# Kernel tuning notes

Hardware: AMD Instinct MI355X
Metric: run time of the kernel (lower is better)

## Reference

```python
import jax, jax.numpy as jnp
import numpy as np

B, L, C = 32, 1024, 32     # batch, seq_len, enc_in
D = 512                     # d_model / hidden_size
SEG = 16                    # seg_len
K = 25                      # moving_avg kernel
SX = L // SEG               # seg_num_x = 64 sequential GRU steps
PRED = 16                   # pred_len == seg_len -> seg_num_y = 1


def setup_inputs() -> dict:
    key = jax.random.key(0)
    ks = jax.random.split(key, 20)
    r = lambda i, shape: jax.random.normal(ks[i], shape, dtype=jnp.float32) * 0.05
    return {
        "x": jax.random.normal(ks[0], (B, L, C), dtype=jnp.float32),
        "W_emb": r(1, (D, SEG)), "b_emb": r(2, (D,)),
        "Wih_s": r(3, (3 * D, D)), "Whh_s": r(4, (3 * D, D)),
        "bih_s": r(5, (3 * D,)), "bhh_s": r(6, (3 * D,)),
        "Wih_t": r(7, (3 * D, D)), "Whh_t": r(8, (3 * D, D)),
        "bih_t": r(9, (3 * D,)), "bhh_t": r(10, (3 * D,)),
        "pos_s": r(11, (1, D // 2)), "ch_s": r(12, (C, D // 2)),
        "pos_t": r(13, (1, D // 2)), "ch_t": r(14, (C, D // 2)),
        "Wps": r(15, (SEG, D)), "bps": r(16, (SEG,)),
        "Wpt": r(17, (SEG, D)), "bpt": r(18, (SEG,)),
    }


def _moving_mean(x, k):
    # Autoformer moving_avg over dim 1 with edge replication (length preserved, k odd)
    pad = (k - 1) // 2
    xp = jnp.concatenate([jnp.repeat(x[:, :1], pad, 1), x, jnp.repeat(x[:, -1:], pad, 1)], axis=1)
    cs = jnp.cumsum(xp, axis=1)
    cs = jnp.concatenate([jnp.zeros_like(cs[:, :1]), cs], axis=1)
    return (cs[:, k:] - cs[:, :-k]) / k


def _gru_cell(x, h, Wih, Whh, bih, bhh):
    gi = x @ Wih.T + bih
    gh = h @ Whh.T + bhh
    ir, iz, in_ = jnp.split(gi, 3, axis=-1)
    hr, hz, hn = jnp.split(gh, 3, axis=-1)
    r = jax.nn.sigmoid(ir + hr)
    z = jax.nn.sigmoid(iz + hz)
    n = jnp.tanh(in_ + r * hn)
    return (1.0 - z) * n + z * h


def _forward(x, W_emb, b_emb, Wih_s, Whh_s, bih_s, bhh_s, Wih_t, Whh_t, bih_t, bhh_t,
             pos_s, ch_s, pos_t, ch_t, Wps, bps, Wpt, bpt):
    seq_last = jax.lax.stop_gradient(x[:, -1:, :])          # (B,1,C), detached
    xc = (x - seq_last).transpose(0, 2, 1)                  # (B,C,L)
    mean = _moving_mean(xc, K)                              # trend
    xs = xc - mean                                          # seasonal residual
    xt = mean
    # value embedding: (B*C, SX, SEG) -> (B*C, SX, D), ReLU
    xs = jax.nn.relu(xs.reshape(-1, SX, SEG) @ W_emb.T + b_emb)
    xt = jax.nn.relu(xt.reshape(-1, SX, SEG) @ W_emb.T + b_emb)
    N = B * C
    h0 = jnp.zeros((N, D), x.dtype)

    def step(carry, inp):
        hs, ht = carry
        xs_i, xt_i = inp
        hs = _gru_cell(xs_i, hs, Wih_s, Whh_s, bih_s, bhh_s)
        ht = _gru_cell(xt_i, ht, Wih_t, Whh_t, bih_t, bhh_t)
        return (hs, ht), None

    (hs, ht), _ = jax.lax.scan(step, (h0, h0), (xs.transpose(1, 0, 2), xt.transpose(1, 0, 2)))

    # decoder (seg_num_y == 1): pos/channel embedding -> one more GRUCell step
    pe_s = jnp.tile(jnp.concatenate([jnp.broadcast_to(pos_s, (C, D // 2)), ch_s], -1), (B, 1))  # (B*C,D)
    pe_t = jnp.tile(jnp.concatenate([jnp.broadcast_to(pos_t, (C, D // 2)), ch_t], -1), (B, 1))
    hs2 = _gru_cell(pe_s, hs, Wih_s, Whh_s, bih_s, bhh_s)
    ht2 = _gru_cell(pe_t, ht, Wih_t, Whh_t, bih_t, bhh_t)
    # predict heads (dropout is identity in eval)
    y = ht2 @ Wpt.T + bpt + hs2 @ Wps.T + bps               # (B*C, SEG)
    y = y.reshape(B, C, PRED).transpose(0, 2, 1)            # (B, PRED, C)
    return y + seq_last


def reference(x, W_emb, b_emb, Wih_s, Whh_s, bih_s, bhh_s, Wih_t, Whh_t, bih_t, bhh_t,
              pos_s, ch_s, pos_t, ch_t, Wps, bps, Wpt, bpt):
    return _forward(x, W_emb, b_emb, Wih_s, Whh_s, bih_s, bhh_s, Wih_t, Whh_t, bih_t, bhh_t,
                    pos_s, ch_s, pos_t, ch_t, Wps, bps, Wpt, bpt)
```

## Files before the change

kernel.cpp:

```cpp
#include <hip/hip_runtime.h>
#include <math.h>

#define B_   32
#define L_   1024
#define C_   32
#define D_   512
#define SEG_ 16
#define SX_  64
#define N_   1024

typedef _Float16 f16x8 __attribute__((ext_vector_type(8)));
typedef _Float16 f16x4 __attribute__((ext_vector_type(4)));
typedef float    f32x4 __attribute__((ext_vector_type(4)));

__device__ __forceinline__ void stage16(const void* g, void* l) {
    __builtin_amdgcn_global_load_lds((const __attribute__((address_space(1))) void*)g,
                                     (__attribute__((address_space(3))) void*)l, 16, 0, 0);
}
__device__ __forceinline__ void stage16l(const void* g, void* l) {
    __builtin_amdgcn_global_load_lds((const __attribute__((address_space(1))) void*)g,
                                     (__attribute__((address_space(3))) void*)l, 16, 0, 1);
}
__device__ __forceinline__ void store_v4_sc0(void* p, f16x8 v) {
    asm volatile("global_store_dwordx4 %0, %1, off sc0" :: "v"(p), "v"(v) : "memory");
}
__device__ __forceinline__ float fsig(float x) {
    return __builtin_amdgcn_rcpf(1.f + __expf(-x));
}
__device__ __forceinline__ float ftanh(float x) {
    return 1.f - 2.f * __builtin_amdgcn_rcpf(1.f + __expf(2.f * x));
}

__global__ __launch_bounds__(256) void prep_kernel(const float* __restrict__ x,
                                                   float* __restrict__ xs_seg,
                                                   float* __restrict__ xt_seg) {
    int b = blockIdx.x >> 2;
    int t = ((blockIdx.x & 3) << 8) + threadIdx.x;
    const float* xb    = x + (size_t)b * (L_ * C_);
    const float* xrow  = xb + (size_t)t * C_;
    const float* xlast = xb + (size_t)(L_ - 1) * C_;

    float diff[C_];
#pragma unroll
    for (int c = 0; c < C_; ++c) diff[c] = xrow[c] - xlast[c];
    float ps[C_ + 1];
    ps[0] = 0.f;
#pragma unroll
    for (int c = 0; c < C_; ++c) ps[c + 1] = ps[c] + diff[c];

    int s = t >> 4, q = t & 15;
#pragma unroll
    for (int c = 0; c < C_; ++c) {
        int lo = c - 12, hi = c + 12;
        float sum = ps[(hi < 31 ? hi : 31) + 1] - ps[lo > 0 ? lo : 0];
        if (lo < 0)  sum += (float)(-lo)     * diff[0];
        if (hi > 31) sum += (float)(hi - 31) * diff[31];
        float mean = sum * (1.0f / 25.0f);
        size_t idx = ((size_t)s * N_ + (size_t)(b * C_ + c)) * SEG_ + q;
        xt_seg[idx] = mean;
        xs_seg[idx] = diff[c] - mean;
    }
}

__global__ __launch_bounds__(256) void emb_kernel(
    const float* __restrict__ xs_seg, const float* __restrict__ xt_seg,
    const float* __restrict__ W_emb, const float* __restrict__ b_emb,
    _Float16* __restrict__ emb_buf, int s0) {
    int bid = blockIdx.x;
    int gru = bid >> 8, sl = (bid >> 4) & 15, nch = bid & 15;
    int step = s0 + sl, n0 = nch * 64;
    const float* xseg = gru ? xt_seg : xs_seg;
    __shared__ float xl[64 * 16];
    int tid = threadIdx.x;
    const float* src = xseg + ((size_t)step * N_ + n0) * SEG_;
    for (int i = tid; i < 1024; i += 256) xl[i] = src[i];

    int kg = tid & 127;
    int rh = tid >> 7;
    float w[4][16], bb[4];
#pragma unroll
    for (int i = 0; i < 4; ++i) {
        int k = kg * 4 + i;
        const float4* wr = (const float4*)(W_emb + (size_t)k * 16);
#pragma unroll
        for (int v = 0; v < 4; ++v) {
            float4 tt = wr[v];
            w[i][v * 4 + 0] = tt.x; w[i][v * 4 + 1] = tt.y;
            w[i][v * 4 + 2] = tt.z; w[i][v * 4 + 3] = tt.w;
        }
        bb[i] = b_emb[k];
    }
    __syncthreads();
    _Float16* dst = emb_buf + ((size_t)(sl * 2 + gru) * N_ + n0) * D_ + kg * 4;
    for (int r = 0; r < 32; ++r) {
        int row = rh * 32 + r;
        float a0 = bb[0], a1 = bb[1], a2 = bb[2], a3 = bb[3];
#pragma unroll
        for (int q = 0; q < 16; ++q) {
            float xv = xl[row * 16 + q];
            a0 = fmaf(xv, w[0][q], a0);
            a1 = fmaf(xv, w[1][q], a1);
            a2 = fmaf(xv, w[2][q], a2);
            a3 = fmaf(xv, w[3][q], a3);
        }
        f16x4 v;
        v[0] = (_Float16)(a0 > 0.f ? a0 : 0.f);
        v[1] = (_Float16)(a1 > 0.f ? a1 : 0.f);
        v[2] = (_Float16)(a2 > 0.f ? a2 : 0.f);
        v[3] = (_Float16)(a3 > 0.f ? a3 : 0.f);
        *(f16x4*)(dst + (size_t)row * D_) = v;
    }
}

__global__ __launch_bounds__(256) void pack_wih_kernel(
    const float* __restrict__ Wih_s, const float* __restrict__ Wih_t,
    _Float16* __restrict__ wp) {
    int e = blockIdx.x * 256 + threadIdx.x;
    int kk = e & 31;
    int t = e >> 5;
    int gc = t % 1536;
    int t2 = t / 1536;
    int kt = t2 & 15, gru = t2 >> 4;
    int member = gc / 192, r = gc % 192;
    int wn = r / 48, r2 = r % 48;
    int gate = r2 >> 4, jl = r2 & 15;
    int j = member * 64 + wn * 16 + jl;
    int k = kt * 32 + kk;
    const float* W = gru ? Wih_t : Wih_s;
    wp[e] = (_Float16)W[(size_t)(gate * 512 + j) * 512 + k];
}

__global__ __launch_bounds__(256) void pack_whh5_kernel(
    const float* __restrict__ Whh_s, const float* __restrict__ Whh_t,
    _Float16* __restrict__ wp) {
    int e = blockIdx.x * 256 + threadIdx.x;
    int fi = e & 7;
    int t = e >> 3;
    int c = t % 3072;
    int t2 = t / 3072;
    int kt = t2 & 3;
    int t3 = t2 >> 2;
    int member = t3 & 7, gru = t3 >> 3;
    int gc = c >> 4, s = c & 15;
    int q = s ^ (gc & 15);
    int k = kt * 128 + q * 8 + fi;
    int wn = gc / 48, r2 = gc % 48;
    int gate = r2 >> 4, jl = r2 & 15;
    int j = member * 64 + wn * 16 + jl;
    const float* W = gru ? Whh_t : Whh_s;
    wp[e] = (_Float16)W[(size_t)(gate * 512 + j) * 512 + k];
}

__global__ __launch_bounds__(256) void pack_pe_kernel(
    const float* __restrict__ pos_s, const float* __restrict__ ch_s,
    const float* __restrict__ pos_t, const float* __restrict__ ch_t,
    _Float16* __restrict__ pe) {
    int e = blockIdx.x * 256 + threadIdx.x;
    int k = e & 511;
    int n = (e >> 9) & 1023;
    int gru = e >> 19;
    int c = n & 31;
    const float* pos = gru ? pos_t : pos_s;
    const float* ch  = gru ? ch_t  : ch_s;
    float v = (k < 256) ? pos[k] : ch[c * 256 + (k - 256)];
    pe[e] = (_Float16)v;
}

__global__ __launch_bounds__(512, 2) void gi_gemm_kernel(
    const _Float16* __restrict__ emb, const _Float16* __restrict__ pe,
    const _Float16* __restrict__ wih_pack,
    _Float16* __restrict__ gi, _Float16* __restrict__ gi_pe, int mode) {
    __shared__ __align__(16) char smem[53248];
    char* sA = smem;
    char* sB = smem + 8192;
    int Mt = blockIdx.x & 7, Nt = blockIdx.x >> 3;
    int sl = blockIdx.y, gru = blockIdx.z;
    int tid = threadIdx.x, w = tid >> 6, lane = tid & 63;
    int wm = w & 1, wn = w >> 1, ml = lane & 15, qq = lane >> 4;

    const char* Ab = mode ? (const char*)(pe  + (size_t)gru * N_ * D_)
                          : (const char*)(emb + (size_t)(sl * 2 + gru) * N_ * D_);
    const char* Bb = (const char*)wih_pack + (size_t)gru * 16 * 1536 * 64
                     + (size_t)Nt * 192 * 64;

    int rA = tid >> 2, kqA = (tid & 3) ^ ((rA >> 1) & 3);
    const char* gA = Ab + (size_t)(Mt * 128 + rA) * 1024 + kqA * 16;
    int g1 = tid >> 2, kq1 = (tid & 3) ^ ((g1 >> 1) & 3);
    int c2 = 512 + tid, g2 = c2 >> 2, kq2 = (c2 & 3) ^ ((g2 >> 1) & 3);

    int offA[4], offB[3];
#pragma unroll
    for (int mf = 0; mf < 4; ++mf) {
        int row = wm * 64 + mf * 16 + ml;
        offA[mf] = (row * 4 + (qq ^ ((row >> 1) & 3))) * 16;
    }
#pragma unroll
    for (int g = 0; g < 3; ++g) {
        int gc = wn * 48 + g * 16 + ml;
        offB[g] = (gc * 4 + (qq ^ ((gc >> 1) & 3))) * 16;
    }

    f32x4 acc[4][3];
#pragma unroll
    for (int mf = 0; mf < 4; ++mf)
#pragma unroll
        for (int g = 0; g < 3; ++g) {
            f32x4 z = {0.f, 0.f, 0.f, 0.f};
            acc[mf][g] = z;
        }

    for (int kt = 0; kt < 16; ++kt) {
        __syncthreads();
        stage16(gA + kt * 64, sA + w * 1024);
        const char* Bkt = Bb + (size_t)kt * (1536 * 64);
        stage16(Bkt + g1 * 64 + kq1 * 16, sB + w * 1024);
        if (w < 4) stage16(Bkt + g2 * 64 + kq2 * 16, sB + 8192 + w * 1024);
        asm volatile("s_waitcnt vmcnt(0)" ::: "memory");
        __syncthreads();
        f16x8 a[4];
#pragma unroll
        for (int mf = 0; mf < 4; ++mf) a[mf] = *(const f16x8*)(sA + offA[mf]);
#pragma unroll
        for (int g = 0; g < 3; ++g) {
            f16x8 b = *(const f16x8*)(sB + offB[g]);
#pragma unroll
            for (int mf = 0; mf < 4; ++mf)
                acc[mf][g] = __builtin_amdgcn_mfma_f32_16x16x32_f16(a[mf], b, acc[mf][g], 0, 0, 0);
        }
    }

    __syncthreads();
#pragma unroll
    for (int mf = 0; mf < 4; ++mf) {
        int wm_c = mf >> 1, rt = mf & 1;
        int tid_c = (wn * 2 + wm_c) * 64 + qq * 16 + ml;
        char* base = smem + wm * 26624 + tid_c * 52;
#pragma unroll
        for (int g = 0; g < 3; ++g)
#pragma unroll
            for (int reg = 0; reg < 4; ++reg) {
                int v = rt * 12 + reg * 3 + g;
                *(_Float16*)(base + v * 2) = (_Float16)acc[mf][g][reg];
            }
    }
    __syncthreads();
    _Float16* ob = mode ? gi_pe + (size_t)gru * 8 * 16 * 512 * 24
                        : gi    + (size_t)(sl * 2 + gru) * 8 * 16 * 512 * 24;
    char* obB = (char*)ob;
#pragma unroll
    for (int s = 0; s < 6; ++s) {
        int o = tid * 16 + s * 8192;
        int mc = o / 24576;
        int o2 = o - mc * 24576;
        int tc = o2 / 48;
        int r  = o2 - tc * 48;
        const char* src = smem + mc * 26624 + tc * 52 + r;
        int4 val;
        val.x = *(const int*)(src);
        val.y = *(const int*)(src + 4);
        val.z = *(const int*)(src + 8);
        val.w = *(const int*)(src + 12);
        *(int4*)(obB + (size_t)(Nt * 16 + Mt * 2 + mc) * 24576 + o2) = val;
    }
}

__global__ __launch_bounds__(512) void gru_chain_kernel(
    const _Float16* __restrict__ whh_pk5,
    const _Float16* __restrict__ gi_base,
    const float* __restrict__ bih_s, const float* __restrict__ bhh_s,
    const float* __restrict__ bih_t, const float* __restrict__ bhh_t,
    _Float16* __restrict__ hbf0, _Float16* __restrict__ hbf1,
    unsigned* __restrict__ flags, int nsteps, int sbase) {
    __shared__ __align__(16) char sA[65536];
    __shared__ __align__(16) char sEx[49152];
    int bid = blockIdx.x;
    int member = bid >> 5, chain = bid & 31;
    int Mt = chain & 15, gru = chain >> 4;
    int tid = threadIdx.x, w = tid >> 6, lane = tid & 63;
    int ml = lane & 15, qq = lane >> 4;
    int km = w & 1, wn = w >> 1;

    const char* h0 = (const char*)hbf0 + ((size_t)gru * N_ + Mt * 64) * 1024;
    const char* h1 = (const char*)hbf1 + ((size_t)gru * N_ + Mt * 64) * 1024;

    f16x8 bfr[3][8];
    {
        const _Float16* Wb = whh_pk5 + (size_t)(gru * 8 + member) * 4 * 24576;
#pragma unroll
        for (int g = 0; g < 3; ++g) {
            int gc = wn * 48 + g * 16 + ml;
#pragma unroll
            for (int ks = 0; ks < 8; ++ks) {
                int kt = km * 2 + (ks >> 2);
                int q8 = ((ks & 3) * 4 + qq) ^ (gc & 15);
                bfr[g][ks] = *(const f16x8*)(Wb + (size_t)kt * 24576
                                             + (size_t)(gc * 16 + q8) * 8);
            }
        }
    }

    int cS0 = (lane & 48) | ((lane & 15) ^ (w & 15));
    int cS1 = (lane & 48) | ((lane & 15) ^ ((w + 8) & 15));

    int offR[4], cp[8];
#pragma unroll
    for (int rt = 0; rt < 4; ++rt) offR[rt] = (rt * 16 + ml) * 1024;
#pragma unroll
    for (int ks = 0; ks < 8; ++ks) {
        int c = km * 32 + ks * 4 + qq;
        cp[ks] = ((c & 48) | ((c & 15) ^ ml)) * 16;
    }

    const float* bi = gru ? bih_t : bih_s;
    const float* bh = gru ? bhh_t : bhh_s;
    int j = member * 64 + wn * 16 + ml;
    float bir = bi[j], biz = bi[D_ + j], bin = bi[2 * D_ + j];
    float bhr = bh[j], bhz = bh[D_ + j], bhn = bh[2 * D_ + j];
    float hp[2][4];
#pragma unroll
    for (int rtL = 0; rtL < 2; ++rtL)
#pragma unroll
        for (int reg = 0; reg < 4; ++reg) {
            int row = Mt * 64 + km * 32 + rtL * 16 + qq * 4 + reg;
            hp[rtL][reg] = (float)hbf0[((size_t)gru * N_ + row) * D_ + j];
        }

    unsigned* fbase = flags + chain * 256;
    const _Float16* giTid0 = gi_base
        + (((size_t)gru * 8 + member) * 16 + Mt) * 512 * 24 + (size_t)tid * 24;
    size_t giStep = (size_t)2 * 8 * 16 * 512 * 24;

    int dir0 = sbase & 1;
    f16x8 gv0, gv1, gv2;
    {
        const _Float16* gp = giTid0;
        gv0 = *(const f16x8*)(gp);
        gv1 = *(const f16x8*)(gp + 8);
        gv2 = *(const f16x8*)(gp + 16);
        const char* hin = dir0 ? h1 : h0;
#pragma unroll
        for (int r = 0; r < 8; ++r) {
            int row = r * 8 + w;
            stage16l(hin + (size_t)row * 1024 + (size_t)((r & 1) ? cS1 : cS0) * 16,
                     sA + row * 1024);
        }
    }

    for (int it = 0; it < nsteps; ++it) {
        int gstep = sbase + it;
        _Float16* hout = (gstep & 1) ? hbf0 : hbf1;

        f32x4 acc[4][3];
#pragma unroll
        for (int rt = 0; rt < 4; ++rt)
#pragma unroll
            for (int g = 0; g < 3; ++g) {
                f32x4 z = {0.f, 0.f, 0.f, 0.f};
                acc[rt][g] = z;
            }

        asm volatile("s_waitcnt vmcnt(0)" ::: "memory");
        __syncthreads();

#pragma unroll
        for (int ks = 0; ks < 8; ++ks) {
            f16x8 a0 = *(const f16x8*)(sA + offR[0] + cp[ks]);
            f16x8 a1 = *(const f16x8*)(sA + offR[1] + cp[ks]);
            f16x8 a2 = *(const f16x8*)(sA + offR[2] + cp[ks]);
            f16x8 a3 = *(const f16x8*)(sA + offR[3] + cp[ks]);
#pragma unroll
            for (int g = 0; g < 3; ++g) {
                acc[0][g] = __builtin_amdgcn_mfma_f32_16x16x32_f16(a0, bfr[g][ks], acc[0][g], 0, 0, 0);
                acc[1][g] = __builtin_amdgcn_mfma_f32_16x16x32_f16(a1, bfr[g][ks], acc[1][g], 0, 0, 0);
                acc[2][g] = __builtin_amdgcn_mfma_f32_16x16x32_f16(a2, bfr[g][ks], acc[2][g], 0, 0, 0);
                acc[3][g] = __builtin_amdgcn_mfma_f32_16x16x32_f16(a3, bfr[g][ks], acc[3][g], 0, 0, 0);
            }
        }

        char* exw = sEx + (size_t)(wn * 64 + lane) * 16;
        if (km == 0) {
#pragma unroll
            for (int g = 0; g < 3; ++g) {
                *(f32x4*)(exw + (size_t)(6 + g) * 4096) = acc[2][g];
                *(f32x4*)(exw + (size_t)(9 + g) * 4096) = acc[3][g];
            }
        } else {
#pragma unroll
            for (int g = 0; g < 3; ++g) {
                *(f32x4*)(exw + (size_t)(0 + g) * 4096) = acc[0][g];
                *(f32x4*)(exw + (size_t)(3 + g) * 4096) = acc[1][g];
            }
        }
        __syncthreads();
        f32x4 s0[3], s1[3];
        if (km == 0) {
#pragma unroll
            for (int g = 0; g < 3; ++g) {
                s0[g] = acc[0][g] + *(const f32x4*)(exw + (size_t)(0 + g) * 4096);
                s1[g] = acc[1][g] + *(const f32x4*)(exw + (size_t)(3 + g) * 4096);
            }
        } else {
#pragma unroll
            for (int g = 0; g < 3; ++g) {
                s0[g] = acc[2][g] + *(const f32x4*)(exw + (size_t)(6 + g) * 4096);
                s1[g] = acc[3][g] + *(const f32x4*)(exw + (size_t)(9 + g) * 4096);
            }
        }

        char* sH = sA;
        int colb = (wn * 16 + ml) * 2;
#pragma unroll
        for (int reg = 0; reg < 4; ++reg) {
            int v0 = reg * 3;
            float gr = (float)((v0 + 0) < 8 ? gv0[(v0 + 0) & 7]
                      : ((v0 + 0) < 16 ? gv1[(v0 + 0) & 7] : gv2[(v0 + 0) & 7]));
            float gz = (float)((v0 + 1) < 8 ? gv0[(v0 + 1) & 7]
                      : ((v0 + 1) < 16 ? gv1[(v0 + 1) & 7] : gv2[(v0 + 1) & 7]));
            float gn = (float)((v0 + 2) < 8 ? gv0[(v0 + 2) & 7]
                      : ((v0 + 2) < 16 ? gv1[(v0 + 2) & 7] : gv2[(v0 + 2) & 7]));
            float r = fsig(s0[0][reg] + gr + bir + bhr);
            float z = fsig(s0[1][reg] + gz + biz + bhz);
            float nn = ftanh(gn + bin + r * (s0[2][reg] + bhn));
            float hv = (1.f - z) * nn + z * hp[0][reg];
            hp[0][reg] = hv;
            int rl = km * 32 + qq * 4 + reg;
            *(_Float16*)(sH + rl * 144 + colb) = (_Float16)hv;
        }
#pragma unroll
        for (int reg = 0; reg < 4; ++reg) {
            int v0 = 12 + reg * 3;
            float gr = (float)((v0 + 0) < 8 ? gv0[(v0 + 0) & 7]
                      : ((v0 + 0) < 16 ? gv1[(v0 + 0) & 7] : gv2[(v0 + 0) & 7]));
            float gz = (float)((v0 + 1) < 8 ? gv0[(v0 + 1) & 7]
                      : ((v0 + 1) < 16 ? gv1[(v0 + 1) & 7] : gv2[(v0 + 1) & 7]));
            float gn = (float)((v0 + 2) < 8 ? gv0[(v0 + 2) & 7]
                      : ((v0 + 2) < 16 ? gv1[(v0 + 2) & 7] : gv2[(v0 + 2) & 7]));
            float r = fsig(s1[0][reg] + gr + bir + bhr);
            float z = fsig(s1[1][reg] + gz + biz + bhz);
            float nn = ftanh(gn + bin + r * (s1[2][reg] + bhn));
            float hv = (1.f - z) * nn + z * hp[1][reg];
            hp[1][reg] = hv;
            int rl = km * 32 + 16 + qq * 4 + reg;
            *(_Float16*)(sH + rl * 144 + colb) = (_Float16)hv;
        }
        __syncthreads();
        {
            int srow = tid >> 3, spart = tid & 7;
            f16x8 hv8 = *(const f16x8*)(sH + srow * 144 + spart * 16);
            _Float16* gdst = hout + ((size_t)gru * N_ + Mt * 64 + srow) * D_
                             + member * 64 + spart * 8;
            store_v4_sc0(gdst, hv8);
        }

        asm volatile("s_waitcnt vmcnt(0)" ::: "memory");
        __syncthreads();
        if (tid == 0)
            __hip_atomic_store(fbase + member * 32, (unsigned)(gstep + 1),
                               __ATOMIC_RELAXED, __HIP_MEMORY_SCOPE_AGENT);

        if (it < nsteps - 1) {
            const _Float16* gp = giTid0 + (size_t)(it + 1) * giStep;
            gv0 = *(const f16x8*)(gp);
            gv1 = *(const f16x8*)(gp + 8);
            gv2 = *(const f16x8*)(gp + 16);
            if (w == 0) {
                const unsigned* fp = fbase + (lane & 7) * 32;
                unsigned tgt = (unsigned)(gstep + 1);
                int guard = 0;
                while (true) {
                    unsigned v = __hip_atomic_load(fp, __ATOMIC_RELAXED,
                                                   __HIP_MEMORY_SCOPE_AGENT);
                    if (__all(v >= tgt)) break;
                    __builtin_amdgcn_s_sleep(1);
                    if (++guard > (1 << 20)) break;
                }
            }
            __syncthreads();
            const char* hinN = ((gstep + 1) & 1) ? h1 : h0;
#pragma unroll
            for (int r = 0; r < 8; ++r) {
                int row = r * 8 + w;
                stage16l(hinN + (size_t)row * 1024 + (size_t)((r & 1) ? cS1 : cS0) * 16,
                         sA + row * 1024);
            }
        }
    }
}

__global__ __launch_bounds__(256) void head_kernel(
    const _Float16* __restrict__ hs2, const _Float16* __restrict__ ht2,
    const float* __restrict__ Wps, const float* __restrict__ bps,
    const float* __restrict__ Wpt, const float* __restrict__ bpt,
    const float* __restrict__ x, float* __restrict__ out) {
    int g = blockIdx.x * 256 + threadIdx.x;
    int n = g >> 4, p = g & 15;
    int b = n >> 5, c = n & 31;
    const _Float16* hs = hs2 + (size_t)n * D_;
    const _Float16* ht = ht2 + (size_t)n * D_;
    const float* ws = Wps + (size_t)p * D_;
    const float* wt = Wpt + (size_t)p * D_;
    float acc = bps[p] + bpt[p];
    for (int k = 0; k < D_; ++k)
        acc += (float)hs[k] * ws[k] + (float)ht[k] * wt[k];
    float last = x[((size_t)b * L_ + (L_ - 1)) * C_ + c];
    out[((size_t)b * SEG_ + p) * C_ + c] = acc + last;
}

extern "C" void kernel_launch(void* const* d_in, const int* in_sizes, int n_in,
                              void* d_out, int out_size, void* d_ws, size_t ws_size,
                              hipStream_t stream) {
    const float* x     = (const float*)d_in[0];
    const float* W_emb = (const float*)d_in[1];
    const float* b_emb = (const float*)d_in[2];
    const float* Wih_s = (const float*)d_in[3];
    const float* Whh_s = (const float*)d_in[4];
    const float* bih_s = (const float*)d_in[5];
    const float* bhh_s = (const float*)d_in[6];
    const float* Wih_t = (const float*)d_in[7];
    const float* Whh_t = (const float*)d_in[8];
    const float* bih_t = (const float*)d_in[9];
    const float* bhh_t = (const float*)d_in[10];
    const float* pos_s = (const float*)d_in[11];
    const float* ch_s  = (const float*)d_in[12];
    const float* pos_t = (const float*)d_in[13];
    const float* ch_t  = (const float*)d_in[14];
    const float* Wps   = (const float*)d_in[15];
    const float* bps   = (const float*)d_in[16];
    const float* Wpt   = (const float*)d_in[17];
    const float* bpt   = (const float*)d_in[18];
    float* out = (float*)d_out;

    char* p = (char*)d_ws;
    float* xs_seg = (float*)p;          p += (size_t)SX_ * N_ * SEG_ * 4;
    float* xt_seg = (float*)p;          p += (size_t)SX_ * N_ * SEG_ * 4;
    _Float16* emb_buf = (_Float16*)p;   p += (size_t)16 * 2 * N_ * D_ * 2;
    _Float16* gi_buf  = (_Float16*)p;   p += (size_t)16 * 2 * 8 * 16 * 512 * 24 * 2;
    _Float16* gi_pe   = (_Float16*)p;   p += (size_t)2 * 8 * 16 * 512 * 24 * 2;
    _Float16* pe_buf  = (_Float16*)p;   p += (size_t)2 * N_ * D_ * 2;
    _Float16* wih_pk  = (_Float16*)p;   p += (size_t)2 * 16 * 1536 * 32 * 2;
    _Float16* whh_pk5 = (_Float16*)p;   p += (size_t)2 * 8 * 4 * 3072 * 8 * 2;
    _Float16* hbf0 = (_Float16*)p;      p += (size_t)2 * N_ * D_ * 2;
    _Float16* hbf1 = (_Float16*)p;      p += (size_t)2 * N_ * D_ * 2;
    unsigned* flags = (unsigned*)p;     p += 32 * 256 * 4;

    hipMemsetAsync(hbf0, 0, (size_t)2 * N_ * D_ * 2, stream);
    hipMemsetAsync(flags, 0, 32 * 256 * 4, stream);

    pack_wih_kernel<<<6144, 256, 0, stream>>>(Wih_s, Wih_t, wih_pk);
    pack_whh5_kernel<<<6144, 256, 0, stream>>>(Whh_s, Whh_t, whh_pk5);
    pack_pe_kernel<<<4096, 256, 0, stream>>>(pos_s, ch_s, pos_t, ch_t, pe_buf);
    prep_kernel<<<B_ * 4, 256, 0, stream>>>(x, xs_seg, xt_seg);

    for (int b = 0; b < 4; ++b) {
        emb_kernel<<<512, 256, 0, stream>>>(xs_seg, xt_seg, W_emb, b_emb, emb_buf, b * 16);
        gi_gemm_kernel<<<dim3(64, 16, 2), 512, 0, stream>>>(
            emb_buf, pe_buf, wih_pk, gi_buf, gi_pe, 0);
        gru_chain_kernel<<<256, 512, 0, stream>>>(
            whh_pk5, gi_buf, bih_s, bhh_s, bih_t, bhh_t,
            hbf0, hbf1, flags, 16, b * 16);
    }
    gi_gemm_kernel<<<dim3(64, 1, 2), 512, 0, stream>>>(
        emb_buf, pe_buf, wih_pk, gi_buf, gi_pe, 1);
    gru_chain_kernel<<<256, 512, 0, stream>>>(
        whh_pk5, gi_pe, bih_s, bhh_s, bih_t, bhh_t,
        hbf0, hbf1, flags, 1, 64);

    head_kernel<<<N_ * SEG_ / 256, 256, 0, stream>>>(
        hbf1, hbf1 + (size_t)N_ * D_, Wps, bps, Wpt, bpt, x, out);
}
```

Baseline: 773.5 us.

## Run all GRU steps in one chain launch and prefetch next-step gate inputs early

New measurement: 773.3 us. About the same (-0.0%).

```diff
diff --git a/kernel.cpp b/kernel.cpp
--- a/kernel.cpp
+++ b/kernel.cpp
@@ -362,6 +362,13 @@
         asm volatile("s_waitcnt vmcnt(0)" ::: "memory");
         __syncthreads();
 
+        int itn = (it + 1 < nsteps) ? it + 1 : it;
+        const _Float16* gpn = giTid0 + (size_t)itn * giStep;
+        f16x8 ngv0 = *(const f16x8*)(gpn);
+        f16x8 ngv1 = *(const f16x8*)(gpn + 8);
+        f16x8 ngv2 = *(const f16x8*)(gpn + 16);
+        __builtin_amdgcn_sched_barrier(0);
+
 #pragma unroll
         for (int ks = 0; ks < 8; ++ks) {
             f16x8 a0 = *(const f16x8*)(sA + offR[0] + cp[ks]);
@@ -459,10 +466,6 @@
                                __ATOMIC_RELAXED, __HIP_MEMORY_SCOPE_AGENT);
 
         if (it < nsteps - 1) {
-            const _Float16* gp = giTid0 + (size_t)(it + 1) * giStep;
-            gv0 = *(const f16x8*)(gp);
-            gv1 = *(const f16x8*)(gp + 8);
-            gv2 = *(const f16x8*)(gp + 16);
             if (w == 0) {
                 const unsigned* fp = fbase + (lane & 7) * 32;
                 unsigned tgt = (unsigned)(gstep + 1);
@@ -484,6 +487,7 @@
                          sA + row * 1024);
             }
         }
+        gv0 = ngv0; gv1 = ngv1; gv2 = ngv2;
     }
 }
 
@@ -530,34 +534,62 @@
     const float* bpt   = (const float*)d_in[18];
     float* out = (float*)d_out;
 
+    const size_t SZ_XS    = (size_t)SX_ * N_ * SEG_ * 4;
+    const size_t SZ_EMB   = (size_t)16 * 2 * N_ * D_ * 2;
+    const size_t SZ_GIB   = (size_t)16 * 2 * 8 * 16 * 512 * 24 * 2;
+    const size_t SZ_GIPE  = (size_t)2 * 8 * 16 * 512 * 24 * 2;
+    const size_t SZ_PE    = (size_t)2 * N_ * D_ * 2;
+    const size_t SZ_WIH   = (size_t)2 * 16 * 1536 * 32 * 2;
+    const size_t SZ_WHH   = (size_t)2 * 8 * 4 * 3072 * 8 * 2;
+    const size_t SZ_H     = (size_t)2 * N_ * D_ * 2;
+    const size_t SZ_FLAGS = 32 * 256 * 4;
+    const size_t fixed = 2 * SZ_XS + SZ_EMB + SZ_GIPE + SZ_PE + SZ_WIH + SZ_WHH
+                         + 2 * SZ_H + SZ_FLAGS;
+    const bool big = ws_size >= fixed + 4 * SZ_GIB;
+    const size_t gi_bytes = big ? 4 * SZ_GIB : SZ_GIB;
+
     char* p = (char*)d_ws;
-    float* xs_seg = (float*)p;          p += (size_t)SX_ * N_ * SEG_ * 4;
-    float* xt_seg = (float*)p;          p += (size_t)SX_ * N_ * SEG_ * 4;
-    _Float16* emb_buf = (_Float16*)p;   p += (size_t)16 * 2 * N_ * D_ * 2;
-    _Float16* gi_buf  = (_Float16*)p;   p += (size_t)16 * 2 * 8 * 16 * 512 * 24 * 2;
-    _Float16* gi_pe   = (_Float16*)p;   p += (size_t)2 * 8 * 16 * 512 * 24 * 2;
-    _Float16* pe_buf  = (_Float16*)p;   p += (size_t)2 * N_ * D_ * 2;
-    _Float16* wih_pk  = (_Float16*)p;   p += (size_t)2 * 16 * 1536 * 32 * 2;
-    _Float16* whh_pk5 = (_Float16*)p;   p += (size_t)2 * 8 * 4 * 3072 * 8 * 2;
-    _Float16* hbf0 = (_Float16*)p;      p += (size_t)2 * N_ * D_ * 2;
-    _Float16* hbf1 = (_Float16*)p;      p += (size_t)2 * N_ * D_ * 2;
-    unsigned* flags = (unsigned*)p;     p += 32 * 256 * 4;
-
-    hipMemsetAsync(hbf0, 0, (size_t)2 * N_ * D_ * 2, stream);
-    hipMemsetAsync(flags, 0, 32 * 256 * 4, stream);
+    float* xs_seg = (float*)p;          p += SZ_XS;
+    float* xt_seg = (float*)p;          p += SZ_XS;
+    _Float16* emb_buf = (_Float16*)p;   p += SZ_EMB;
+    _Float16* gi_buf  = (_Float16*)p;   p += gi_bytes;
+    _Float16* gi_pe   = (_Float16*)p;   p += SZ_GIPE;
+    _Float16* pe_buf  = (_Float16*)p;   p += SZ_PE;
+    _Float16* wih_pk  = (_Float16*)p;   p += SZ_WIH;
+    _Float16* whh_pk5 = (_Float16*)p;   p += SZ_WHH;
+    _Float16* hbf0 = (_Float16*)p;      p += SZ_H;
+    _Float16* hbf1 = (_Float16*)p;      p += SZ_H;
+    unsigned* flags = (unsigned*)p;     p += SZ_FLAGS;
+
+    hipMemsetAsync(hbf0, 0, SZ_H, stream);
+    hipMemsetAsync(flags, 0, SZ_FLAGS, stream);
 
     pack_wih_kernel<<<6144, 256, 0, stream>>>(Wih_s, Wih_t, wih_pk);
     pack_whh5_kernel<<<6144, 256, 0, stream>>>(Whh_s, Whh_t, whh_pk5);
     pack_pe_kernel<<<4096, 256, 0, stream>>>(pos_s, ch_s, pos_t, ch_t, pe_buf);
     prep_kernel<<<B_ * 4, 256, 0, stream>>>(x, xs_seg, xt_seg);
 
-    for (int b = 0; b < 4; ++b) {
-        emb_kernel<<<512, 256, 0, stream>>>(xs_seg, xt_seg, W_emb, b_emb, emb_buf, b * 16);
-        gi_gemm_kernel<<<dim3(64, 16, 2), 512, 0, stream>>>(
-            emb_buf, pe_buf, wih_pk, gi_buf, gi_pe, 0);
+    const size_t giBatchElems = (size_t)16 * 2 * 8 * 16 * 512 * 24;
+    if (big) {
+        for (int b = 0; b < 4; ++b) {
+            emb_kernel<<<512, 256, 0, stream>>>(xs_seg, xt_seg, W_emb, b_emb,
+                                                emb_buf, b * 16);
+            gi_gemm_kernel<<<dim3(64, 16, 2), 512, 0, stream>>>(
+                emb_buf, pe_buf, wih_pk, gi_buf + (size_t)b * giBatchElems, gi_pe, 0);
+        }
         gru_chain_kernel<<<256, 512, 0, stream>>>(
             whh_pk5, gi_buf, bih_s, bhh_s, bih_t, bhh_t,
-            hbf0, hbf1, flags, 16, b * 16);
+            hbf0, hbf1, flags, 64, 0);
+    } else {
+        for (int b = 0; b < 4; ++b) {
+            emb_kernel<<<512, 256, 0, stream>>>(xs_seg, xt_seg, W_emb, b_emb,
+                                                emb_buf, b * 16);
+            gi_gemm_kernel<<<dim3(64, 16, 2), 512, 0, stream>>>(
+                emb_buf, pe_buf, wih_pk, gi_buf, gi_pe, 0);
+            gru_chain_kernel<<<256, 512, 0, stream>>>(
+                whh_pk5, gi_buf, bih_s, bhh_s, bih_t, bhh_t,
+                hbf0, hbf1, flags, 16, b * 16);
+        }
     }
     gi_gemm_kernel<<<dim3(64, 1, 2), 512, 0, stream>>>(
         emb_buf, pe_buf, wih_pk, gi_buf, gi_pe, 1);
```
